# Performance work log

Measured on AMD Instinct MI355X. Metric: run time of the kernel, lower is better.

## Reference

```python
import jax, jax.numpy as jnp
import numpy as np

S, B, D, H, F = 2048, 2, 1024, 16, 4096
HD = D // H
EPS = 1e-5


def setup_inputs() -> dict:
    key = jax.random.key(0)
    ks = jax.random.split(key, 16)
    sc_d = 1.0 / np.sqrt(D)
    sc_f = 1.0 / np.sqrt(F)
    return {
        "src": jax.random.normal(ks[0], (S, B, D), jnp.float32),
        # attention projections: Linear weights stored as [in, out] (y = x @ W + b)
        "Wq": jax.random.normal(ks[1], (D, D), jnp.float32) * sc_d,
        "bq": jnp.zeros((D,), jnp.float32),
        "Wk": jax.random.normal(ks[2], (D, D), jnp.float32) * sc_d,
        "bk": jnp.zeros((D,), jnp.float32),
        "Wv": jax.random.normal(ks[3], (D, D), jnp.float32) * sc_d,
        "bv": jnp.zeros((D,), jnp.float32),
        "Wo": jax.random.normal(ks[4], (D, D), jnp.float32) * sc_d,
        "bo": jnp.zeros((D,), jnp.float32),
        # norm1
        "g1": jnp.ones((D,), jnp.float32),
        "be1": jnp.zeros((D,), jnp.float32),
        # FFN
        "W1": jax.random.normal(ks[5], (D, F), jnp.float32) * sc_d,
        "bf1": jnp.zeros((F,), jnp.float32),
        "W2": jax.random.normal(ks[6], (F, D), jnp.float32) * sc_f,
        "bf2": jnp.zeros((D,), jnp.float32),
        # norm2
        "g2": jnp.ones((D,), jnp.float32),
        "be2": jnp.zeros((D,), jnp.float32),
    }


def _layernorm(x, g, b):
    m = jnp.mean(x, axis=-1, keepdims=True)
    v = jnp.mean(jnp.square(x - m), axis=-1, keepdims=True)
    return (x - m) * jax.lax.rsqrt(v + EPS) * g + b


def reference(src, Wq, bq, Wk, bk, Wv, bv, Wo, bo, g1, be1, W1, bf1, W2, bf2, g2, be2):
    # --- self attention (dropout_p=0 / eval mode => dropouts are identity) ---
    scaling = float(HD) ** -0.5
    q = (src @ Wq + bq) * scaling            # [S,B,D]
    k = src @ Wk + bk
    v = src @ Wv + bv
    # split heads: torch view(S, B*H, hd) == reshape(S, B, H, hd)
    qh = q.reshape(S, B, H, HD)
    kh = k.reshape(S, B, H, HD)
    vh = v.reshape(S, B, H, HD)
    scores = jnp.einsum("sbhd,tbhd->bhst", qh, kh)      # [B,H,S,S]
    attn = jax.nn.softmax(scores, axis=-1)
    ctx = jnp.einsum("bhst,tbhd->sbhd", attn, vh).reshape(S, B, D)
    attn_out = ctx @ Wo + bo
    # residual + norm1
    x = _layernorm(src + attn_out, g1, be1)
    # FFN (ReLU)
    ff = jax.nn.relu(x @ W1 + bf1) @ W2 + bf2
    # residual + norm2
    return _layernorm(x + ff, g2, be2)
```

## Files before the change

### kernel.cpp

```cpp
#include <hip/hip_runtime.h>
#include <hip/hip_bf16.h>

#define S_  2048
#define B_  2
#define D_  1024
#define H_  16
#define F_  4096
#define HD_ 64
#define NT_ (S_*B_)

typedef __attribute__((ext_vector_type(8))) short short8;
typedef __attribute__((ext_vector_type(4))) short short4v;
typedef __attribute__((ext_vector_type(4))) float f32x4;

#define MFMA16x16x32(a,b,c) __builtin_amdgcn_mfma_f32_16x16x32_bf16((a),(b),(c),0,0,0)

#define AS1C(p) ((const __attribute__((address_space(1))) void*)(p))
#define AS3(p)  ((__attribute__((address_space(3))) void*)(p))

__device__ __forceinline__ short f2b(float f) {
  union { float f; unsigned u; } x; x.f = f;
  unsigned r = x.u + 0x7FFFu + ((x.u >> 16) & 1u);
  return (short)(r >> 16);
}
__device__ __forceinline__ float b2f(short u) {
  union { unsigned u; float f; } x; x.u = ((unsigned)(unsigned short)u) << 16;
  return x.f;
}
__device__ __forceinline__ unsigned cvtpk(float a, float b) {
  unsigned r;
  asm("v_cvt_pk_bf16_f32 %0, %1, %2" : "=v"(r) : "v"(a), "v"(b));
  return r;
}
__device__ __forceinline__ float exp2fast(float x) {
  float r;
  asm("v_exp_f32 %0, %1" : "=v"(r) : "v"(x));
  return r;
}

__global__ __launch_bounds__(256) void to_bf16_k(const float* __restrict__ in,
                                                 short* __restrict__ out) {
  int i = (blockIdx.x * 256 + threadIdx.x) * 8;
  float4 a = *(const float4*)(in + i);
  float4 b = *(const float4*)(in + i + 4);
  short8 o;
  o[0] = f2b(a.x); o[1] = f2b(a.y); o[2] = f2b(a.z); o[3] = f2b(a.w);
  o[4] = f2b(b.x); o[5] = f2b(b.y); o[6] = f2b(b.z); o[7] = f2b(b.w);
  *(short8*)(out + i) = o;
}

__global__ __launch_bounds__(256) void transpose_to_bf16(const float* __restrict__ W,
                                                         short* __restrict__ Wt,
                                                         int K, int N, int colbase, int outK) {
  __shared__ short t[32][33];
  int tx = threadIdx.x & 31, ty = threadIdx.x >> 5;
  int kbase = blockIdx.y * 32, nbase = blockIdx.x * 32;
#pragma unroll
  for (int yy = 0; yy < 4; ++yy) {
    int kk = ty + yy * 8;
    t[kk][tx] = f2b(W[(size_t)(kbase + kk) * N + nbase + tx]);
  }
  __syncthreads();
#pragma unroll
  for (int yy = 0; yy < 4; ++yy) {
    int nn = ty + yy * 8;
    Wt[(size_t)(nbase + nn + colbase) * outK + kbase + tx] = t[tx][nn];
  }
}

template<int MODE>
__global__ __launch_bounds__(256, 2) void gemm_bt(
    const short* __restrict__ A, const short* __restrict__ Bt,
    int M, int N, int K, int lda,
    const float* __restrict__ bias0, const float* __restrict__ bias1,
    const float* __restrict__ bias2,
    float* __restrict__ outf,
    short* __restrict__ outq, short* __restrict__ outk, short* __restrict__ outv) {
  __shared__ __align__(16) short As[128 * 64];
  __shared__ __align__(16) short Bs[128 * 64];
  int tid = threadIdx.x;
  int lane = tid & 63, w = tid >> 6;
  int g = lane >> 4, r = lane & 15;
  int wm = w >> 1, wn = w & 1;

  int gx = gridDim.x, gy = gridDim.y;
  int nwg = gx * gy * gridDim.z;
  int flat = (blockIdx.z * gy + blockIdx.y) * gx + blockIdx.x;
  int cpx = nwg >> 3;
  int swz = (flat & 7) * cpx + (flat >> 3);
  int z = swz / (gx * gy);
  int rem = swz - z * gx * gy;
  int row0 = (rem / gx) * 128;
  int col0 = (rem % gx) * 128;
  size_t koff = (size_t)z * K;

  f32x4 acc[4][4];
#pragma unroll
  for (int m = 0; m < 4; ++m)
#pragma unroll
    for (int n = 0; n < 4; ++n) acc[m][n] = (f32x4){0.f, 0.f, 0.f, 0.f};

  for (int kt = 0; kt < K; kt += 64) {
#pragma unroll
    for (int p = 0; p < 4; ++p) {
      int idx = tid + p * 256;
      int row = idx >> 3, c = idx & 7;
      int scol = ((c ^ (row & 7)) << 3);
      __builtin_amdgcn_global_load_lds(AS1C(A  + (size_t)(row0 + row) * lda + koff + kt + scol),
                                       AS3(As + idx * 8), 16, 0, 0);
      __builtin_amdgcn_global_load_lds(AS1C(Bt + (size_t)(col0 + row) * lda + koff + kt + scol),
                                       AS3(Bs + idx * 8), 16, 0, 0);
    }
    __syncthreads();
    short8 af[4][2], bfr[4][2];
#pragma unroll
    for (int m = 0; m < 4; ++m)
#pragma unroll
      for (int kk = 0; kk < 2; ++kk) {
        int row = wm * 64 + m * 16 + r;
        af[m][kk] = *(const short8*)(As + row * 64 + (((kk * 4 + g) ^ (r & 7)) << 3));
      }
#pragma unroll
    for (int n = 0; n < 4; ++n)
#pragma unroll
      for (int kk = 0; kk < 2; ++kk) {
        int row = wn * 64 + n * 16 + r;
        bfr[n][kk] = *(const short8*)(Bs + row * 64 + (((kk * 4 + g) ^ (r & 7)) << 3));
      }
#pragma unroll
    for (int m = 0; m < 4; ++m)
#pragma unroll
      for (int n = 0; n < 4; ++n)
#pragma unroll
        for (int kk = 0; kk < 2; ++kk)
          acc[m][n] = MFMA16x16x32(af[m][kk], bfr[n][kk], acc[m][n]);
    __syncthreads();
  }

  int rb = row0 + wm * 64, cb = col0 + wn * 64;
#pragma unroll
  for (int m = 0; m < 4; ++m) {
#pragma unroll
    for (int n = 0; n < 4; ++n) {
#pragma unroll
      for (int j = 0; j < 4; ++j) {
        int row = rb + m * 16 + g * 4 + j;
        int col = cb + n * 16 + r;
        float v = acc[m][n][j];
        if (MODE == 0) {
          int s = row >> 1, b = row & 1;
          if (col < 1024) {
            float q = (v + bias0[col]) * (0.125f * 1.44269504088896f);
            int h = col >> 6, hd = col & 63;
            outq[((size_t)(b * H_ + h) * S_ + s) * HD_ + hd] = f2b(q);
          } else if (col < 2048) {
            int c2 = col - 1024;
            float kk = v + bias1[c2];
            int h = c2 >> 6, hd = c2 & 63;
            outk[((size_t)(b * H_ + h) * S_ + s) * HD_ + hd] = f2b(kk);
          } else {
            int c2 = col - 2048;
            float vv = v + bias2[c2];
            int h = c2 >> 6, hd = c2 & 63;
            outv[((size_t)(b * H_ + h) * HD_ + hd) * S_ + s] = f2b(vv);
          }
        } else if (MODE == 2) {
          size_t o = (size_t)row * N + col;
          float t = v + bias0[col];
          outq[o] = f2b(t > 0.f ? t : 0.f);
        } else {
          outf[(size_t)z * M * N + (size_t)row * N + col] = v;
        }
      }
    }
  }
}

__global__ __launch_bounds__(256, 4) void flash_attn(const short* __restrict__ Q,
                                                     const short* __restrict__ Kb,
                                                     const short* __restrict__ Vt,
                                                     short* __restrict__ ctx) {
  __shared__ __align__(16) short Ks[2][64 * 64];
  __shared__ __align__(16) short Vs[2][64 * 64];
  __shared__ __align__(16) short P[4][16][64];
  int tid = threadIdx.x;
  int lane = tid & 63, w = tid >> 6;
  int g = lane >> 4, r = lane & 15;
  int f = blockIdx.x;
  int xcd = f & 7, loc = f >> 3;
  int bh = xcd * 4 + (loc >> 5);
  int qt = loc & 31;
  const short* qp = Q  + (size_t)bh * S_ * HD_;
  const short* kp = Kb + (size_t)bh * S_ * HD_;
  const short* vp = Vt + (size_t)bh * HD_ * S_;
  int q0 = qt * 64 + w * 16;

  short8 qf[2];
#pragma unroll
  for (int kk = 0; kk < 2; ++kk)
    qf[kk] = *(const short8*)(qp + (size_t)(q0 + r) * HD_ + kk * 32 + g * 8);

  f32x4 acc[4];
  float mi = -1e30f, li = 0.f;
#pragma unroll
  for (int db = 0; db < 4; ++db) acc[db] = (f32x4){0.f, 0.f, 0.f, 0.f};

#pragma unroll
  for (int p = 0; p < 2; ++p) {
    int idx = tid + p * 256;
    int row = idx >> 3, c = idx & 7;
    int scol = ((c ^ (row & 7)) << 3);
    __builtin_amdgcn_global_load_lds(AS1C(kp + (size_t)row * HD_ + scol),
                                     AS3(&Ks[0][0] + idx * 8), 16, 0, 0);
    __builtin_amdgcn_global_load_lds(AS1C(vp + (size_t)row * S_ + scol),
                                     AS3(&Vs[0][0] + idx * 8), 16, 0, 0);
  }
  __syncthreads();

  int cur = 0;
  for (int t = 0; t < S_ / 64; ++t) {
    if (t + 1 < S_ / 64) {
      int kv1 = (t + 1) * 64;
#pragma unroll
      for (int p = 0; p < 2; ++p) {
        int idx = tid + p * 256;
        int row = idx >> 3, c = idx & 7;
        int scol = ((c ^ (row & 7)) << 3);
        __builtin_amdgcn_global_load_lds(AS1C(kp + (size_t)(kv1 + row) * HD_ + scol),
                                         AS3(&Ks[cur ^ 1][0] + idx * 8), 16, 0, 0);
        __builtin_amdgcn_global_load_lds(AS1C(vp + (size_t)row * S_ + kv1 + scol),
                                         AS3(&Vs[cur ^ 1][0] + idx * 8), 16, 0, 0);
      }
    }
    const short* Kc = &Ks[cur][0];
    const short* Vc = &Vs[cur][0];
    short8 kf[4][2];
#pragma unroll
    for (int kb = 0; kb < 4; ++kb)
#pragma unroll
      for (int kk = 0; kk < 2; ++kk) {
        int row = kb * 16 + r;
        kf[kb][kk] = *(const short8*)(Kc + row * 64 + (((kk * 4 + g) ^ (r & 7)) << 3));
      }

    f32x4 st[4];
#pragma unroll
    for (int kb = 0; kb < 4; ++kb) {
      f32x4 tt = (f32x4){0.f, 0.f, 0.f, 0.f};
      tt = MFMA16x16x32(kf[kb][0], qf[0], tt);
      tt = MFMA16x16x32(kf[kb][1], qf[1], tt);
      st[kb] = tt;
    }

    float pm = st[0][0];
#pragma unroll
    for (int kb = 0; kb < 4; ++kb)
#pragma unroll
      for (int j = 0; j < 4; ++j) pm = fmaxf(pm, st[kb][j]);
    pm = fmaxf(pm, __shfl_xor(pm, 16));
    pm = fmaxf(pm, __shfl_xor(pm, 32));
    if (!__all(pm <= mi + 8.0f)) {
      float mn = fmaxf(mi, pm);
      float sc = exp2fast(mi - mn);
      mi = mn;
      li *= sc;
#pragma unroll
      for (int db = 0; db < 4; ++db)
#pragma unroll
        for (int j = 0; j < 4; ++j) acc[db][j] *= sc;
    }
    float rs = 0.f;
#pragma unroll
    for (int kb = 0; kb < 4; ++kb)
#pragma unroll
      for (int j = 0; j < 4; ++j) {
        float p0 = exp2fast(st[kb][j] - mi);
        st[kb][j] = p0;
        rs += p0;
      }
    rs += __shfl_xor(rs, 16);
    rs += __shfl_xor(rs, 32);
    li += rs;

#pragma unroll
    for (int kb = 0; kb < 4; ++kb) {
      unsigned w0 = cvtpk(st[kb][0], st[kb][1]);
      unsigned w1 = cvtpk(st[kb][2], st[kb][3]);
      unsigned long long pw = (unsigned long long)w0 | ((unsigned long long)w1 << 32);
      int col = (kb * 16 + g * 4) ^ ((r & 7) << 3);
      *(unsigned long long*)(&P[w][r][0] + col) = pw;
    }

    short8 vf[4][2];
#pragma unroll
    for (int db = 0; db < 4; ++db)
#pragma unroll
      for (int ks = 0; ks < 2; ++ks) {
        int row = db * 16 + r;
        vf[db][ks] = *(const short8*)(Vc + row * 64 + (((ks * 4 + g) ^ (r & 7)) << 3));
      }
    short8 pf[2];
#pragma unroll
    for (int ks = 0; ks < 2; ++ks) {
      int col = (ks * 32 + g * 8) ^ ((r & 7) << 3);
      pf[ks] = *(const short8*)(&P[w][r][0] + col);
    }

#pragma unroll
    for (int db = 0; db < 4; ++db) {
      acc[db] = MFMA16x16x32(vf[db][0], pf[0], acc[db]);
      acc[db] = MFMA16x16x32(vf[db][1], pf[1], acc[db]);
    }

    __syncthreads();
    cur ^= 1;
  }

  int b = bh >> 4, h = bh & 15;
  float inv = 1.0f / li;
  int s = q0 + r;
  int token = s * B_ + b;
#pragma unroll
  for (int db = 0; db < 4; ++db) {
    unsigned w0 = cvtpk(acc[db][0] * inv, acc[db][1] * inv);
    unsigned w1 = cvtpk(acc[db][2] * inv, acc[db][3] * inv);
    unsigned long long pw = (unsigned long long)w0 | ((unsigned long long)w1 << 32);
    *(unsigned long long*)(ctx + (size_t)token * D_ + h * 64 + db * 16 + g * 4) = pw;
  }
}

template<int RESBF16, int WF, int WB>
__global__ __launch_bounds__(256) void layernorm_fused(
    const float* __restrict__ p0, const float* __restrict__ p1,
    const float* __restrict__ bias,
    const float* __restrict__ residf, const short* __restrict__ residb,
    const float* __restrict__ gm, const float* __restrict__ bt,
    float* __restrict__ of, short* __restrict__ ob) {
  __shared__ float r1[4], r2[4];
  int row = blockIdx.x, tid = threadIdx.x;
  size_t base = (size_t)row * D_ + tid * 4;
  float4 a = *(const float4*)(p0 + base);
  float4 b = *(const float4*)(p1 + base);
  float4 bi = *(const float4*)(bias + tid * 4);
  float4 v;
  if (RESBF16) {
    short4v rb = *(const short4v*)(residb + base);
    v.x = a.x + b.x + bi.x + b2f(rb[0]);
    v.y = a.y + b.y + bi.y + b2f(rb[1]);
    v.z = a.z + b.z + bi.z + b2f(rb[2]);
    v.w = a.w + b.w + bi.w + b2f(rb[3]);
  } else {
    float4 rf = *(const float4*)(residf + base);
    v.x = a.x + b.x + bi.x + rf.x;
    v.y = a.y + b.y + bi.y + rf.y;
    v.z = a.z + b.z + bi.z + rf.z;
    v.w = a.w + b.w + bi.w + rf.w;
  }
  float s1 = v.x + v.y + v.z + v.w;
  float s2 = v.x * v.x + v.y * v.y + v.z * v.z + v.w * v.w;
#pragma unroll
  for (int off = 32; off > 0; off >>= 1) {
    s1 += __shfl_xor(s1, off, 64);
    s2 += __shfl_xor(s2, off, 64);
  }
  int wid = tid >> 6;
  if ((tid & 63) == 0) { r1[wid] = s1; r2[wid] = s2; }
  __syncthreads();
  s1 = r1[0] + r1[1] + r1[2] + r1[3];
  s2 = r2[0] + r2[1] + r2[2] + r2[3];
  float mean = s1 * (1.0f / D_);
  float var = s2 * (1.0f / D_) - mean * mean;
  float rstd = rsqrtf(var + 1e-5f);
  float4 gv = *(const float4*)(gm + tid * 4);
  float4 bv = *(const float4*)(bt + tid * 4);
  float o0 = (v.x - mean) * rstd * gv.x + bv.x;
  float o1 = (v.y - mean) * rstd * gv.y + bv.y;
  float o2 = (v.z - mean) * rstd * gv.z + bv.z;
  float o3 = (v.w - mean) * rstd * gv.w + bv.w;
  if (WF) *(float4*)(of + base) = make_float4(o0, o1, o2, o3);
  if (WB) {
    short4v o;
    o[0] = f2b(o0); o[1] = f2b(o1); o[2] = f2b(o2); o[3] = f2b(o3);
    *(short4v*)(ob + base) = o;
  }
}

extern "C" void kernel_launch(void* const* d_in, const int* in_sizes, int n_in,
                              void* d_out, int out_size, void* d_ws, size_t ws_size,
                              hipStream_t stream) {
  const float* src = (const float*)d_in[0];
  const float* Wq  = (const float*)d_in[1];
  const float* bq  = (const float*)d_in[2];
  const float* Wk  = (const float*)d_in[3];
  const float* bk  = (const float*)d_in[4];
  const float* Wv  = (const float*)d_in[5];
  const float* bv  = (const float*)d_in[6];
  const float* Wo  = (const float*)d_in[7];
  const float* bo  = (const float*)d_in[8];
  const float* g1  = (const float*)d_in[9];
  const float* be1 = (const float*)d_in[10];
  const float* W1  = (const float*)d_in[11];
  const float* bf1 = (const float*)d_in[12];
  const float* W2  = (const float*)d_in[13];
  const float* bf2 = (const float*)d_in[14];
  const float* g2  = (const float*)d_in[15];
  const float* be2 = (const float*)d_in[16];
  float* out = (float*)d_out;
  char* ws = (char*)d_ws;

  const size_t MiB = 1024 * 1024;
  short* Wqkv_t = (short*)(ws + 0 * MiB);
  short* Wo_t   = (short*)(ws + 6 * MiB);
  short* W1_t   = (short*)(ws + 8 * MiB);
  short* W2_t   = (short*)(ws + 16 * MiB);
  short* xb     = (short*)(ws + 24 * MiB);
  short* x1b    = (short*)(ws + 24 * MiB);
  short* ctx    = (short*)(ws + 32 * MiB);
  short* qb_    = (short*)(ws + 40 * MiB);
  short* kb_    = (short*)(ws + 48 * MiB);
  short* vb_    = (short*)(ws + 56 * MiB);
  short* hid    = (short*)(ws + 32 * MiB);
  float* part   = (float*)(ws + 64 * MiB);
  float* part1  = part + (size_t)NT_ * D_;

  to_bf16_k<<<2048, 256, 0, stream>>>(src, xb);

  transpose_to_bf16<<<dim3(32, 32),  256, 0, stream>>>(Wq, Wqkv_t, 1024, 1024, 0,    1024);
  transpose_to_bf16<<<dim3(32, 32),  256, 0, stream>>>(Wk, Wqkv_t, 1024, 1024, 1024, 1024);
  transpose_to_bf16<<<dim3(32, 32),  256, 0, stream>>>(Wv, Wqkv_t, 1024, 1024, 2048, 1024);
  transpose_to_bf16<<<dim3(32, 32),  256, 0, stream>>>(Wo, Wo_t,   1024, 1024, 0,    1024);
  transpose_to_bf16<<<dim3(128, 32), 256, 0, stream>>>(W1, W1_t,   1024, 4096, 0,    1024);
  transpose_to_bf16<<<dim3(32, 128), 256, 0, stream>>>(W2, W2_t,   4096, 1024, 0,    4096);

  gemm_bt<0><<<dim3(24, 32, 1), 256, 0, stream>>>(xb, Wqkv_t, NT_, 3072, 1024, 1024,
                                                  bq, bk, bv, nullptr, qb_, kb_, vb_);
  flash_attn<<<1024, 256, 0, stream>>>(qb_, kb_, vb_, ctx);
  gemm_bt<3><<<dim3(8, 32, 2), 256, 0, stream>>>(ctx, Wo_t, NT_, 1024, 512, 1024,
                                                 nullptr, nullptr, nullptr, part,
                                                 nullptr, nullptr, nullptr);
  layernorm_fused<0, 0, 1><<<NT_, 256, 0, stream>>>(part, part1, bo, src, nullptr,
                                                    g1, be1, nullptr, x1b);
  gemm_bt<2><<<dim3(32, 32, 1), 256, 0, stream>>>(x1b, W1_t, NT_, 4096, 1024, 1024,
                                                  bf1, nullptr, nullptr, nullptr,
                                                  hid, nullptr, nullptr);
  gemm_bt<3><<<dim3(8, 32, 2), 256, 0, stream>>>(hid, W2_t, NT_, 1024, 2048, 4096,
                                                 nullptr, nullptr, nullptr, part,
                                                 nullptr, nullptr, nullptr);
  layernorm_fused<1, 1, 0><<<NT_, 256, 0, stream>>>(part, part1, bf2, nullptr, x1b,
                                                    g2, be2, out, nullptr);
}
```

Baseline: 240.2 us.

## Double-buffer GEMM LDS tiles and raise wave priority around attention MFMAs

The GEMM kernel now keeps two LDS buffers each for A and B. It issues the global-to-LDS loads for the next K tile before computing on the current one, so memory latency can overlap with MFMA work instead of stalling at a barrier every iteration. Shared memory per block doubles, which may limit occupancy. The attention kernel also wraps its QK and PV MFMA blocks in s_setprio so waves issuing matrix ops get scheduling priority.

After: 275.5 us. 14.7% more time.

```diff
diff --git a/kernel.cpp b/kernel.cpp
--- a/kernel.cpp
+++ b/kernel.cpp
@@ -76,8 +76,8 @@
     const float* __restrict__ bias2,
     float* __restrict__ outf,
     short* __restrict__ outq, short* __restrict__ outk, short* __restrict__ outv) {
-  __shared__ __align__(16) short As[128 * 64];
-  __shared__ __align__(16) short Bs[128 * 64];
+  __shared__ __align__(16) short As[2][128 * 64];
+  __shared__ __align__(16) short Bs[2][128 * 64];
   int tid = threadIdx.x;
   int lane = tid & 63, w = tid >> 6;
   int g = lane >> 4, r = lane & 15;
@@ -94,38 +94,52 @@
   int col0 = (rem % gx) * 128;
   size_t koff = (size_t)z * K;
 
+  const short* Abase = A  + (size_t)row0 * lda + koff;
+  const short* Bbase = Bt + (size_t)col0 * lda + koff;
+
   f32x4 acc[4][4];
 #pragma unroll
   for (int m = 0; m < 4; ++m)
 #pragma unroll
     for (int n = 0; n < 4; ++n) acc[m][n] = (f32x4){0.f, 0.f, 0.f, 0.f};
 
+#define GEMM_STAGE(BUF, KT)                                                            \
+  {                                                                                    \
+    _Pragma("unroll")                                                                  \
+    for (int p = 0; p < 4; ++p) {                                                      \
+      int idx = tid + p * 256;                                                         \
+      int row = idx >> 3, c = idx & 7;                                                 \
+      int scol = ((c ^ (row & 7)) << 3);                                               \
+      __builtin_amdgcn_global_load_lds(AS1C(Abase + (size_t)row * lda + (KT) + scol),  \
+                                       AS3(&As[BUF][0] + idx * 8), 16, 0, 0);          \
+      __builtin_amdgcn_global_load_lds(AS1C(Bbase + (size_t)row * lda + (KT) + scol),  \
+                                       AS3(&Bs[BUF][0] + idx * 8), 16, 0, 0);          \
+    }                                                                                  \
+  }
+
+  GEMM_STAGE(0, 0);
+  __syncthreads();
+
+  int cur = 0;
   for (int kt = 0; kt < K; kt += 64) {
-#pragma unroll
-    for (int p = 0; p < 4; ++p) {
-      int idx = tid + p * 256;
-      int row = idx >> 3, c = idx & 7;
-      int scol = ((c ^ (row & 7)) << 3);
-      __builtin_amdgcn_global_load_lds(AS1C(A  + (size_t)(row0 + row) * lda + koff + kt + scol),
-                                       AS3(As + idx * 8), 16, 0, 0);
-      __builtin_amdgcn_global_load_lds(AS1C(Bt + (size_t)(col0 + row) * lda + koff + kt + scol),
-                                       AS3(Bs + idx * 8), 16, 0, 0);
-    }
-    __syncthreads();
+    if (kt + 64 < K) GEMM_STAGE(cur ^ 1, kt + 64);
+
+    const short* Ac = &As[cur][0];
+    const short* Bc = &Bs[cur][0];
     short8 af[4][2], bfr[4][2];
 #pragma unroll
     for (int m = 0; m < 4; ++m)
 #pragma unroll
       for (int kk = 0; kk < 2; ++kk) {
         int row = wm * 64 + m * 16 + r;
-        af[m][kk] = *(const short8*)(As + row * 64 + (((kk * 4 + g) ^ (r & 7)) << 3));
+        af[m][kk] = *(const short8*)(Ac + row * 64 + (((kk * 4 + g) ^ (r & 7)) << 3));
       }
 #pragma unroll
     for (int n = 0; n < 4; ++n)
 #pragma unroll
       for (int kk = 0; kk < 2; ++kk) {
         int row = wn * 64 + n * 16 + r;
-        bfr[n][kk] = *(const short8*)(Bs + row * 64 + (((kk * 4 + g) ^ (r & 7)) << 3));
+        bfr[n][kk] = *(const short8*)(Bc + row * 64 + (((kk * 4 + g) ^ (r & 7)) << 3));
       }
 #pragma unroll
     for (int m = 0; m < 4; ++m)
@@ -134,8 +148,11 @@
 #pragma unroll
         for (int kk = 0; kk < 2; ++kk)
           acc[m][n] = MFMA16x16x32(af[m][kk], bfr[n][kk], acc[m][n]);
+
     __syncthreads();
-  }
+    cur ^= 1;
+  }
+#undef GEMM_STAGE
 
   int rb = row0 + wm * 64, cb = col0 + wn * 64;
 #pragma unroll
@@ -244,6 +261,7 @@
       }
 
     f32x4 st[4];
+    __builtin_amdgcn_s_setprio(1);
 #pragma unroll
     for (int kb = 0; kb < 4; ++kb) {
       f32x4 tt = (f32x4){0.f, 0.f, 0.f, 0.f};
@@ -251,6 +269,7 @@
       tt = MFMA16x16x32(kf[kb][1], qf[1], tt);
       st[kb] = tt;
     }
+    __builtin_amdgcn_s_setprio(0);
 
     float pm = st[0][0];
 #pragma unroll
@@ -306,11 +325,13 @@
       pf[ks] = *(const short8*)(&P[w][r][0] + col);
     }
 
+    __builtin_amdgcn_s_setprio(1);
 #pragma unroll
     for (int db = 0; db < 4; ++db) {
       acc[db] = MFMA16x16x32(vf[db][0], pf[0], acc[db]);
       acc[db] = MFMA16x16x32(vf[db][1], pf[1], acc[db]);
     }
+    __builtin_amdgcn_s_setprio(0);
 
     __syncthreads();
     cur ^= 1;
```
